# Kernel optimization log

Measured on AMD Instinct MI355X. Metric: run time of the kernel, lower is better.

The kernel has to match this reference:

```python
import jax, jax.numpy as jnp
import numpy as np

B = 32768      # batch size
D = 256        # embedding dim
C = 2048       # number of classes (label range)
WEIGHT = 1.0
TEMPERATURE = 0.3
EPS = 1e-12


def setup_inputs() -> dict:
    key = jax.random.key(0)
    k1, k2 = jax.random.split(key)
    features = jax.random.normal(k1, (B, D), dtype=jnp.float32)
    labels = jax.random.randint(k2, (B,), 0, C, dtype=jnp.int32)
    return {"features": features, "labels": labels, "epoch": 5}


def reference(features, labels, epoch):
    # L2-normalize embeddings (F.normalize, p=2, dim=1)
    norms = jnp.sqrt(jnp.sum(features * features, axis=1, keepdims=True))
    f = features / jnp.maximum(norms, EPS)                      # [B, D]

    # per-class segment sums / counts (vectorized replacement of the python loop)
    ones = jnp.ones((f.shape[0],), dtype=f.dtype)
    counts = jax.ops.segment_sum(ones, labels, num_segments=C)  # [C]
    sums = jax.ops.segment_sum(f, labels, num_segments=C)       # [C, D]
    centroids = sums / jnp.maximum(counts, 1.0)[:, None]        # [C, D] (mean; empty classes masked later)

    # leave-one-out positive centroid: (sum_class - f_i) / (n_class - 1)
    cnt_i = counts[labels]                                       # [B]
    c_p = (sums[labels] - f) / jnp.maximum(cnt_i - 1.0, 1.0)[:, None]
    d_p = jnp.sqrt(jnp.sum((f - c_p) ** 2, axis=1) + EPS)        # [B]

    # distances to all class centroids: ||f||=1 after normalization
    cn2 = jnp.sum(centroids * centroids, axis=1)                 # [C]
    d2 = 1.0 + cn2[None, :] - 2.0 * (f @ centroids.T)           # [B, C]
    d = jnp.sqrt(jnp.maximum(d2, EPS))

    # mask own class and empty (absent-in-batch) classes, take min negative distance
    class_ids = jnp.arange(C, dtype=labels.dtype)
    neg_mask = (counts[None, :] > 0) & (labels[:, None] != class_ids[None, :])
    d_n = jnp.min(jnp.where(neg_mask, d, jnp.inf), axis=1)       # [B]

    # samples are skipped if their class is a singleton or no negative class exists
    valid = (cnt_i > 1.0) & jnp.isfinite(d_n)
    d_n_safe = jnp.where(jnp.isfinite(d_n), d_n, 0.0)

    # temperature schedule: min(temperature + 0.02*epoch, 1)
    temp = min(TEMPERATURE + 0.02 * epoch, 1.0)

    # ln(1 + exp((d_p - d_n)/t)) == softplus
    loss_per_sample = jax.nn.softplus((d_p - d_n_safe) / temp)
    cnt = jnp.sum(valid.astype(f.dtype))
    loss = jnp.where(cnt > 0,
                     jnp.sum(jnp.where(valid, loss_per_sample, 0.0)) / jnp.maximum(cnt, 1.0),
                     0.0)
    return WEIGHT * loss
```

## Files before the change

### kernel.cpp

```cpp
#include <hip/hip_runtime.h>
#include <hip/hip_bf16.h>
#include <math.h>

constexpr int Bn = 32768;
constexpr int Dn = 256;
constexpr int Cn = 2048;
constexpr int NSPLIT = 4;
constexpr int CLS_PER_BLK = Cn / NSPLIT;
constexpr int NIT = CLS_PER_BLK / 16;
#define EPSF 1e-12f
#define INFF __builtin_inff()

typedef __bf16 bf16x8 __attribute__((ext_vector_type(8)));
typedef __bf16 bf16x4 __attribute__((ext_vector_type(4)));
typedef float  f32x4  __attribute__((ext_vector_type(4)));

__device__ inline void async_copy16(const void* g, void* l) {
    __builtin_amdgcn_global_load_lds(
        (const __attribute__((address_space(1))) void*)g,
        (__attribute__((address_space(3))) void*)l, 16, 0, 0);
}

__global__ __launch_bounds__(256) void k_prep(const float* __restrict__ feat,
                                              const int* __restrict__ labels,
                                              __bf16* __restrict__ fneg,
                                              int* __restrict__ hist) {
    const int wave = threadIdx.x >> 6, lane = threadIdx.x & 63;
    const int s = blockIdx.x * 4 + wave;
    const float4 v = ((const float4*)(feat + (size_t)s * Dn))[lane];
    float ss = v.x * v.x + v.y * v.y + v.z * v.z + v.w * v.w;
    #pragma unroll
    for (int off = 1; off < 64; off <<= 1) ss += __shfl_xor(ss, off, 64);
    const float inv = -2.0f / fmaxf(sqrtf(ss), EPSF);
    bf16x4 bf;
    bf[0] = (__bf16)(v.x * inv); bf[1] = (__bf16)(v.y * inv);
    bf[2] = (__bf16)(v.z * inv); bf[3] = (__bf16)(v.w * inv);
    *(bf16x4*)(fneg + (size_t)s * Dn + lane * 4) = bf;
    if (lane == 0) atomicAdd(&hist[labels[s]], 1);
}

__global__ __launch_bounds__(256) void k_scan(const int* __restrict__ hist,
                                              int* __restrict__ cnt_i,
                                              int* __restrict__ offs,
                                              int* __restrict__ offs_work) {
    __shared__ int part[256];
    const int t = threadIdx.x;
    int h[8], pre[8]; int sum = 0;
    #pragma unroll
    for (int j = 0; j < 8; ++j) { h[j] = hist[t * 8 + j]; pre[j] = sum; sum += h[j]; }
    int v = sum;
    part[t] = v; __syncthreads();
    for (int off = 1; off < 256; off <<= 1) {
        int add = (t >= off) ? part[t - off] : 0;
        __syncthreads();
        v += add; part[t] = v;
        __syncthreads();
    }
    const int base = v - sum;
    #pragma unroll
    for (int j = 0; j < 8; ++j) {
        const int b = t * 8 + j, o = base + pre[j];
        cnt_i[b] = h[j]; offs[b] = o; offs_work[b] = o;
    }
}

__global__ __launch_bounds__(256) void k_scatter(const int* __restrict__ labels,
                                                 int* __restrict__ offs_work,
                                                 int* __restrict__ order) {
    const int i = blockIdx.x * 256 + threadIdx.x;
    const int pos = atomicAdd(&offs_work[labels[i]], 1);
    order[pos] = i;
}

__global__ __launch_bounds__(256) void k_centseg(const __bf16* __restrict__ fneg,
                                                 const int* __restrict__ order,
                                                 const int* __restrict__ offs,
                                                 const int* __restrict__ cnt_i,
                                                 __bf16* __restrict__ centK,
                                                 float* __restrict__ cn2x) {
    const int wave = threadIdx.x >> 6, lane = threadIdx.x & 63;
    const int c = blockIdx.x * 4 + wave;
    const int n = cnt_i[c], start = offs[c];
    int myidx = 0;
    if (lane < n) myidx = order[start + lane];
    float sx = 0.f, sy = 0.f, sz = 0.f, sw = 0.f;
    const int nf = (n < 64) ? n : 64;
    for (int j = 0; j < nf; ++j) {
        const int idx = __shfl(myidx, j, 64);
        const bf16x4 v = *(const bf16x4*)(fneg + (size_t)idx * Dn + lane * 4);
        sx += -0.5f * (float)v[0]; sy += -0.5f * (float)v[1];
        sz += -0.5f * (float)v[2]; sw += -0.5f * (float)v[3];
    }
    for (int j = 64; j < n; ++j) {
        const int idx = order[start + j];
        const bf16x4 v = *(const bf16x4*)(fneg + (size_t)idx * Dn + lane * 4);
        sx += -0.5f * (float)v[0]; sy += -0.5f * (float)v[1];
        sz += -0.5f * (float)v[2]; sw += -0.5f * (float)v[3];
    }
    const float invn = 1.0f / fmaxf((float)n, 1.0f);
    const float cx = sx * invn, cy = sy * invn, cz = sz * invn, cw = sw * invn;
    bf16x4 cb; cb[0] = (__bf16)cx; cb[1] = (__bf16)cy; cb[2] = (__bf16)cz; cb[3] = (__bf16)cw;
    *(bf16x4*)(centK + ((size_t)(lane >> 1) * Cn + c) * 8 + (lane & 1) * 4) = cb;
    float ss = cx * cx + cy * cy + cz * cz + cw * cw;
    #pragma unroll
    for (int off = 1; off < 64; off <<= 1) ss += __shfl_xor(ss, off, 64);
    if (lane == 0) cn2x[c] = (n > 0) ? ss : INFF;
}

__global__ __launch_bounds__(256, 2) void k_main(const __bf16* __restrict__ fneg,
                                                 const int* __restrict__ labels,
                                                 const __bf16* __restrict__ centK,
                                                 const float* __restrict__ cn2x,
                                                 float* __restrict__ minval,
                                                 float* __restrict__ dotown) {
    __shared__ __align__(16) __bf16 sB[2][16 * Dn];
    __shared__ float s_cn2[CLS_PER_BLK];
    const int lane = threadIdx.x & 63, wave = threadIdx.x >> 6;
    const int m16 = lane & 15, quad = lane >> 4;
    const int sbase = blockIdx.x * 256 + wave * 64;
    const int c_begin = blockIdx.y * CLS_PER_BLK;

    bf16x8 a[4][8];
    #pragma unroll
    for (int p = 0; p < 4; ++p) {
        const __bf16* fr = fneg + (size_t)(sbase + p * 16 + m16) * Dn + quad * 8;
        #pragma unroll
        for (int t = 0; t < 8; ++t) a[p][t] = *(const bf16x8*)(fr + t * 32);
    }
    int lab[4][4];
    #pragma unroll
    for (int p = 0; p < 4; ++p)
        #pragma unroll
        for (int r = 0; r < 4; ++r)
            lab[p][r] = labels[sbase + p * 16 + quad * 4 + r];

    float rm[4][4], dacc[4][4];
    #pragma unroll
    for (int p = 0; p < 4; ++p)
        #pragma unroll
        for (int r = 0; r < 4; ++r) { rm[p][r] = INFF; dacc[p][r] = 0.0f; }

    auto stage = [&](int buf, int it) {
        const int c0 = c_begin + it * 16;
        #pragma unroll
        for (int j = 0; j < 2; ++j) {
            const int chunk = wave * 128 + j * 64 + lane;
            const int kc = chunk >> 4, n = chunk & 15;
            const __bf16* g = centK + ((size_t)kc * Cn + (c0 + n)) * 8;
            __bf16* l = &sB[buf][(size_t)(wave * 128 + j * 64) * 8];
            async_copy16(g, l);
        }
    };

    stage(0, 0);
    for (int c = threadIdx.x; c < CLS_PER_BLK; c += 256) s_cn2[c] = cn2x[c_begin + c];
    __syncthreads();
    for (int it = 0; it < NIT; ++it) {
        const int cur = it & 1;
        if (it + 1 < NIT) stage(cur ^ 1, it + 1);
        const float cn2v = s_cn2[it * 16 + m16];
        const __bf16* ls = &sB[cur][0];
        f32x4 acc[4] = {{0.f,0.f,0.f,0.f},{0.f,0.f,0.f,0.f},
                        {0.f,0.f,0.f,0.f},{0.f,0.f,0.f,0.f}};
        #pragma unroll
        for (int t = 0; t < 8; ++t) {
            const bf16x8 b = *(const bf16x8*)(ls + t * 512 + lane * 8);
            #pragma unroll
            for (int p = 0; p < 4; ++p)
                acc[p] = __builtin_amdgcn_mfma_f32_16x16x32_bf16(a[p][t], b, acc[p], 0, 0, 0);
        }
        const int crow = c_begin + it * 16 + m16;
        #pragma unroll
        for (int p = 0; p < 4; ++p)
            #pragma unroll
            for (int r = 0; r < 4; ++r) {
                const bool own = (crow == lab[p][r]);
                const float sel = own ? INFF : cn2v;
                rm[p][r] = fminf(rm[p][r], sel + acc[p][r]);
                dacc[p][r] += own ? acc[p][r] : 0.0f;
            }
        __syncthreads();
    }
    #pragma unroll
    for (int off = 1; off < 16; off <<= 1)
        #pragma unroll
        for (int p = 0; p < 4; ++p)
            #pragma unroll
            for (int r = 0; r < 4; ++r) {
                rm[p][r] = fminf(rm[p][r], __shfl_xor(rm[p][r], off, 64));
                dacc[p][r] += __shfl_xor(dacc[p][r], off, 64);
            }
    if (m16 == 0) {
        float* mv = minval + (size_t)blockIdx.y * Bn;
        float* dv = dotown + (size_t)blockIdx.y * Bn;
        #pragma unroll
        for (int p = 0; p < 4; ++p)
            #pragma unroll
            for (int r = 0; r < 4; ++r) {
                mv[sbase + p * 16 + quad * 4 + r] = rm[p][r];
                dv[sbase + p * 16 + quad * 4 + r] = dacc[p][r];
            }
    }
}

__global__ __launch_bounds__(256) void k_final(const int* __restrict__ labels,
                                               const int* __restrict__ cnt_i,
                                               const float* __restrict__ cn2x,
                                               const float* __restrict__ minval,
                                               const float* __restrict__ dotown,
                                               const int* __restrict__ epoch,
                                               float* __restrict__ accum) {
    const int i = blockIdx.x * 256 + threadIdx.x;
    const int lane = threadIdx.x & 63;
    const float temp = fminf(0.3f + 0.02f * (float)(*epoch), 1.0f);
    float m = minval[i];
    float draw = dotown[i];
    #pragma unroll
    for (int k = 1; k < NSPLIT; ++k) {
        m = fminf(m, minval[(size_t)k * Bn + i]);
        draw += dotown[(size_t)k * Bn + i];
    }
    const int l = labels[i];
    const int n = cnt_i[l];
    const float nf = (float)n;
    const float cn2 = cn2x[l];
    const float fds = nf * (-0.5f * draw);
    const float fm1 = fmaxf(nf - 1.0f, 1.0f);
    const float fdcp = (fds - 1.0f) / fm1;
    const float cp2 = (nf * nf * cn2 - 2.0f * fds + 1.0f) / (fm1 * fm1);
    const float dp2 = 1.0f - 2.0f * fdcp + cp2;
    const float d_p = sqrtf(fmaxf(dp2, 0.0f) + EPSF);
    const bool finite = (m < 1e37f);
    const float d_n = finite ? sqrtf(fmaxf(1.0f + m, EPSF)) : 0.0f;
    const bool valid = (n > 1) && finite;
    const float x = (d_p - d_n) / temp;
    const float sp = fmaxf(x, 0.0f) + log1pf(expf(-fabsf(x)));
    float ws = valid ? sp : 0.0f, wc = valid ? 1.0f : 0.0f;
    #pragma unroll
    for (int off = 1; off < 64; off <<= 1) {
        ws += __shfl_xor(ws, off, 64);
        wc += __shfl_xor(wc, off, 64);
    }
    if (lane == 0) {
        atomicAdd(&accum[0], ws);
        atomicAdd(&accum[1], wc);
    }
}

__global__ void k_out(const float* __restrict__ accum, float* __restrict__ out) {
    const float s = accum[0], c = accum[1];
    out[0] = (c > 0.0f) ? (s / fmaxf(c, 1.0f)) : 0.0f;
}

extern "C" void kernel_launch(void* const* d_in, const int* in_sizes, int n_in,
                              void* d_out, int out_size, void* d_ws, size_t ws_size,
                              hipStream_t stream) {
    const float* feat  = (const float*)d_in[0];
    const int* labels  = (const int*)d_in[1];
    const int* epoch   = (const int*)d_in[2];
    float* out = (float*)d_out;
    char* ws = (char*)d_ws;

    size_t off = 0;
    __bf16* fneg     = (__bf16*)(ws + off); off += (size_t)Bn * Dn * 2;
    __bf16* centK    = (__bf16*)(ws + off); off += (size_t)Cn * Dn * 2;
    float*  cn2x     = (float*)(ws + off);  off += (size_t)Cn * 4;
    int*    hist     = (int*)(ws + off);    off += (size_t)Cn * 4;
    int*    cnt_i    = (int*)(ws + off);    off += (size_t)Cn * 4;
    int*    offs     = (int*)(ws + off);    off += (size_t)Cn * 4;
    int*    offs_wk  = (int*)(ws + off);    off += (size_t)Cn * 4;
    int*    order    = (int*)(ws + off);    off += (size_t)Bn * 4;
    float*  minval   = (float*)(ws + off);  off += (size_t)NSPLIT * Bn * 4;
    float*  dotown   = (float*)(ws + off);  off += (size_t)NSPLIT * Bn * 4;
    float*  accum    = (float*)(ws + off);  off += 2 * 4;

    (void)hipMemsetAsync(hist,  0, (size_t)Cn * sizeof(int), stream);
    (void)hipMemsetAsync(accum, 0, 2 * sizeof(float), stream);

    k_prep<<<Bn / 4, 256, 0, stream>>>(feat, labels, fneg, hist);
    k_scan<<<1, 256, 0, stream>>>(hist, cnt_i, offs, offs_wk);
    k_scatter<<<Bn / 256, 256, 0, stream>>>(labels, offs_wk, order);
    k_centseg<<<Cn / 4, 256, 0, stream>>>(fneg, order, offs, cnt_i, centK, cn2x);
    dim3 g5(Bn / 256, NSPLIT);
    k_main<<<g5, 256, 0, stream>>>(fneg, labels, centK, cn2x, minval, dotown);
    k_final<<<Bn / 256, 256, 0, stream>>>(labels, cnt_i, cn2x, minval, dotown,
                                          epoch, accum);
    k_out<<<1, 1, 0, stream>>>(accum, out);
}
```

Measured before the change: 166.2 us.

## Fuse all stages into one cooperative persistent kernel with grid syncs

Replaces the chain of seven kernel launches and two memsets with a single cooperative kernel. The stages are normalize, scan, scatter, centroid, distance GEMM and final reduction, and grid-wide barriers separate them. NSPLIT is also raised to 8 so the persistent grid has more GEMM work units to spread out. This removes launch gaps but adds the cost of grid syncs, and the single-block scan stage leaves the rest of the grid idle. The GEMM stage's occupancy is also limited by the cooperative grid size.

```diff
diff --git a/kernel.cpp b/kernel.cpp
--- a/kernel.cpp
+++ b/kernel.cpp
@@ -1,13 +1,17 @@
 #include <hip/hip_runtime.h>
 #include <hip/hip_bf16.h>
+#include <hip/hip_cooperative_groups.h>
 #include <math.h>
+
+namespace cg = cooperative_groups;
 
 constexpr int Bn = 32768;
 constexpr int Dn = 256;
 constexpr int Cn = 2048;
-constexpr int NSPLIT = 4;
+constexpr int NSPLIT = 8;
 constexpr int CLS_PER_BLK = Cn / NSPLIT;
 constexpr int NIT = CLS_PER_BLK / 16;
+constexpr int NU = (Bn / 256) * NSPLIT;
 #define EPSF 1e-12f
 #define INFF __builtin_inff()
 
@@ -21,235 +25,236 @@
         (__attribute__((address_space(3))) void*)l, 16, 0, 0);
 }
 
-__global__ __launch_bounds__(256) void k_prep(const float* __restrict__ feat,
-                                              const int* __restrict__ labels,
-                                              __bf16* __restrict__ fneg,
-                                              int* __restrict__ hist) {
-    const int wave = threadIdx.x >> 6, lane = threadIdx.x & 63;
-    const int s = blockIdx.x * 4 + wave;
-    const float4 v = ((const float4*)(feat + (size_t)s * Dn))[lane];
-    float ss = v.x * v.x + v.y * v.y + v.z * v.z + v.w * v.w;
-    #pragma unroll
-    for (int off = 1; off < 64; off <<= 1) ss += __shfl_xor(ss, off, 64);
-    const float inv = -2.0f / fmaxf(sqrtf(ss), EPSF);
-    bf16x4 bf;
-    bf[0] = (__bf16)(v.x * inv); bf[1] = (__bf16)(v.y * inv);
-    bf[2] = (__bf16)(v.z * inv); bf[3] = (__bf16)(v.w * inv);
-    *(bf16x4*)(fneg + (size_t)s * Dn + lane * 4) = bf;
-    if (lane == 0) atomicAdd(&hist[labels[s]], 1);
-}
-
-__global__ __launch_bounds__(256) void k_scan(const int* __restrict__ hist,
-                                              int* __restrict__ cnt_i,
-                                              int* __restrict__ offs,
-                                              int* __restrict__ offs_work) {
-    __shared__ int part[256];
-    const int t = threadIdx.x;
-    int h[8], pre[8]; int sum = 0;
-    #pragma unroll
-    for (int j = 0; j < 8; ++j) { h[j] = hist[t * 8 + j]; pre[j] = sum; sum += h[j]; }
-    int v = sum;
-    part[t] = v; __syncthreads();
-    for (int off = 1; off < 256; off <<= 1) {
-        int add = (t >= off) ? part[t - off] : 0;
-        __syncthreads();
-        v += add; part[t] = v;
-        __syncthreads();
-    }
-    const int base = v - sum;
-    #pragma unroll
-    for (int j = 0; j < 8; ++j) {
-        const int b = t * 8 + j, o = base + pre[j];
-        cnt_i[b] = h[j]; offs[b] = o; offs_work[b] = o;
-    }
-}
-
-__global__ __launch_bounds__(256) void k_scatter(const int* __restrict__ labels,
-                                                 int* __restrict__ offs_work,
-                                                 int* __restrict__ order) {
-    const int i = blockIdx.x * 256 + threadIdx.x;
-    const int pos = atomicAdd(&offs_work[labels[i]], 1);
-    order[pos] = i;
-}
-
-__global__ __launch_bounds__(256) void k_centseg(const __bf16* __restrict__ fneg,
-                                                 const int* __restrict__ order,
-                                                 const int* __restrict__ offs,
-                                                 const int* __restrict__ cnt_i,
-                                                 __bf16* __restrict__ centK,
-                                                 float* __restrict__ cn2x) {
-    const int wave = threadIdx.x >> 6, lane = threadIdx.x & 63;
-    const int c = blockIdx.x * 4 + wave;
-    const int n = cnt_i[c], start = offs[c];
-    int myidx = 0;
-    if (lane < n) myidx = order[start + lane];
-    float sx = 0.f, sy = 0.f, sz = 0.f, sw = 0.f;
-    const int nf = (n < 64) ? n : 64;
-    for (int j = 0; j < nf; ++j) {
-        const int idx = __shfl(myidx, j, 64);
-        const bf16x4 v = *(const bf16x4*)(fneg + (size_t)idx * Dn + lane * 4);
-        sx += -0.5f * (float)v[0]; sy += -0.5f * (float)v[1];
-        sz += -0.5f * (float)v[2]; sw += -0.5f * (float)v[3];
-    }
-    for (int j = 64; j < n; ++j) {
-        const int idx = order[start + j];
-        const bf16x4 v = *(const bf16x4*)(fneg + (size_t)idx * Dn + lane * 4);
-        sx += -0.5f * (float)v[0]; sy += -0.5f * (float)v[1];
-        sz += -0.5f * (float)v[2]; sw += -0.5f * (float)v[3];
-    }
-    const float invn = 1.0f / fmaxf((float)n, 1.0f);
-    const float cx = sx * invn, cy = sy * invn, cz = sz * invn, cw = sw * invn;
-    bf16x4 cb; cb[0] = (__bf16)cx; cb[1] = (__bf16)cy; cb[2] = (__bf16)cz; cb[3] = (__bf16)cw;
-    *(bf16x4*)(centK + ((size_t)(lane >> 1) * Cn + c) * 8 + (lane & 1) * 4) = cb;
-    float ss = cx * cx + cy * cy + cz * cz + cw * cw;
-    #pragma unroll
-    for (int off = 1; off < 64; off <<= 1) ss += __shfl_xor(ss, off, 64);
-    if (lane == 0) cn2x[c] = (n > 0) ? ss : INFF;
-}
-
-__global__ __launch_bounds__(256, 2) void k_main(const __bf16* __restrict__ fneg,
-                                                 const int* __restrict__ labels,
-                                                 const __bf16* __restrict__ centK,
-                                                 const float* __restrict__ cn2x,
-                                                 float* __restrict__ minval,
-                                                 float* __restrict__ dotown) {
+__global__ __launch_bounds__(256, 2) void k_fused(
+    const float* __restrict__ feat, const int* __restrict__ labels,
+    const int* __restrict__ epoch,
+    __bf16* fneg, int* hist, int* cnt_i, int* offs, int* offs_wk, int* order,
+    __bf16* centK, float* cn2x, float* minval, float* dotown,
+    float* accum, float* out)
+{
     __shared__ __align__(16) __bf16 sB[2][16 * Dn];
     __shared__ float s_cn2[CLS_PER_BLK];
-    const int lane = threadIdx.x & 63, wave = threadIdx.x >> 6;
+    __shared__ int s_part[256];
+
+    cg::grid_group gg = cg::this_grid();
+    const int tid = threadIdx.x;
+    const int gtid = blockIdx.x * 256 + tid;
+    const int nthreads = gridDim.x * 256;
+    const int nwaves = nthreads >> 6;
+    const int wave_id = gtid >> 6;
+    const int lane = tid & 63;
+    const int wave = tid >> 6;
+
+    for (int c = gtid; c < Cn; c += nthreads) hist[c] = 0;
+    if (gtid < 2) accum[gtid] = 0.0f;
+    gg.sync();
+
+    for (int s = wave_id; s < Bn; s += nwaves) {
+        const float4 v = ((const float4*)(feat + (size_t)s * Dn))[lane];
+        float ss = v.x * v.x + v.y * v.y + v.z * v.z + v.w * v.w;
+        #pragma unroll
+        for (int off = 1; off < 64; off <<= 1) ss += __shfl_xor(ss, off, 64);
+        const float inv = -2.0f / fmaxf(sqrtf(ss), EPSF);
+        bf16x4 bf;
+        bf[0] = (__bf16)(v.x * inv); bf[1] = (__bf16)(v.y * inv);
+        bf[2] = (__bf16)(v.z * inv); bf[3] = (__bf16)(v.w * inv);
+        *(bf16x4*)(fneg + (size_t)s * Dn + lane * 4) = bf;
+        if (lane == 0) atomicAdd(&hist[labels[s]], 1);
+    }
+    gg.sync();
+
+    if (blockIdx.x == 0) {
+        int h[8], pre[8]; int sum = 0;
+        #pragma unroll
+        for (int j = 0; j < 8; ++j) { h[j] = hist[tid * 8 + j]; pre[j] = sum; sum += h[j]; }
+        int v = sum;
+        s_part[tid] = v; __syncthreads();
+        for (int off = 1; off < 256; off <<= 1) {
+            int add = (tid >= off) ? s_part[tid - off] : 0;
+            __syncthreads();
+            v += add; s_part[tid] = v;
+            __syncthreads();
+        }
+        const int base = v - sum;
+        #pragma unroll
+        for (int j = 0; j < 8; ++j) {
+            const int b = tid * 8 + j, o = base + pre[j];
+            cnt_i[b] = h[j]; offs[b] = o; offs_wk[b] = o;
+        }
+    }
+    gg.sync();
+
+    for (int i = gtid; i < Bn; i += nthreads) {
+        const int pos = atomicAdd(&offs_wk[labels[i]], 1);
+        order[pos] = i;
+    }
+    gg.sync();
+
+    for (int c = wave_id; c < Cn; c += nwaves) {
+        const int n = cnt_i[c], start = offs[c];
+        int myidx = 0;
+        if (lane < n) myidx = order[start + lane];
+        float sx = 0.f, sy = 0.f, sz = 0.f, sw = 0.f;
+        const int nf = (n < 64) ? n : 64;
+        for (int j = 0; j < nf; ++j) {
+            const int idx = __shfl(myidx, j, 64);
+            const bf16x4 v = *(const bf16x4*)(fneg + (size_t)idx * Dn + lane * 4);
+            sx += -0.5f * (float)v[0]; sy += -0.5f * (float)v[1];
+            sz += -0.5f * (float)v[2]; sw += -0.5f * (float)v[3];
+        }
+        for (int j = 64; j < n; ++j) {
+            const int idx = order[start + j];
+            const bf16x4 v = *(const bf16x4*)(fneg + (size_t)idx * Dn + lane * 4);
+            sx += -0.5f * (float)v[0]; sy += -0.5f * (float)v[1];
+            sz += -0.5f * (float)v[2]; sw += -0.5f * (float)v[3];
+        }
+        const float invn = 1.0f / fmaxf((float)n, 1.0f);
+        const float cx = sx * invn, cy = sy * invn, cz = sz * invn, cw = sw * invn;
+        bf16x4 cb; cb[0] = (__bf16)cx; cb[1] = (__bf16)cy;
+        cb[2] = (__bf16)cz; cb[3] = (__bf16)cw;
+        *(bf16x4*)(centK + ((size_t)(lane >> 1) * Cn + c) * 8 + (lane & 1) * 4) = cb;
+        float ss = cx * cx + cy * cy + cz * cz + cw * cw;
+        #pragma unroll
+        for (int off = 1; off < 64; off <<= 1) ss += __shfl_xor(ss, off, 64);
+        if (lane == 0) cn2x[c] = (n > 0) ? ss : INFF;
+    }
+    gg.sync();
+
     const int m16 = lane & 15, quad = lane >> 4;
-    const int sbase = blockIdx.x * 256 + wave * 64;
-    const int c_begin = blockIdx.y * CLS_PER_BLK;
-
-    bf16x8 a[4][8];
-    #pragma unroll
-    for (int p = 0; p < 4; ++p) {
-        const __bf16* fr = fneg + (size_t)(sbase + p * 16 + m16) * Dn + quad * 8;
-        #pragma unroll
-        for (int t = 0; t < 8; ++t) a[p][t] = *(const bf16x8*)(fr + t * 32);
-    }
-    int lab[4][4];
-    #pragma unroll
-    for (int p = 0; p < 4; ++p)
-        #pragma unroll
-        for (int r = 0; r < 4; ++r)
-            lab[p][r] = labels[sbase + p * 16 + quad * 4 + r];
-
-    float rm[4][4], dacc[4][4];
-    #pragma unroll
-    for (int p = 0; p < 4; ++p)
-        #pragma unroll
-        for (int r = 0; r < 4; ++r) { rm[p][r] = INFF; dacc[p][r] = 0.0f; }
-
-    auto stage = [&](int buf, int it) {
-        const int c0 = c_begin + it * 16;
-        #pragma unroll
-        for (int j = 0; j < 2; ++j) {
-            const int chunk = wave * 128 + j * 64 + lane;
-            const int kc = chunk >> 4, n = chunk & 15;
-            const __bf16* g = centK + ((size_t)kc * Cn + (c0 + n)) * 8;
-            __bf16* l = &sB[buf][(size_t)(wave * 128 + j * 64) * 8];
-            async_copy16(g, l);
-        }
-    };
-
-    stage(0, 0);
-    for (int c = threadIdx.x; c < CLS_PER_BLK; c += 256) s_cn2[c] = cn2x[c_begin + c];
-    __syncthreads();
-    for (int it = 0; it < NIT; ++it) {
-        const int cur = it & 1;
-        if (it + 1 < NIT) stage(cur ^ 1, it + 1);
-        const float cn2v = s_cn2[it * 16 + m16];
-        const __bf16* ls = &sB[cur][0];
-        f32x4 acc[4] = {{0.f,0.f,0.f,0.f},{0.f,0.f,0.f,0.f},
-                        {0.f,0.f,0.f,0.f},{0.f,0.f,0.f,0.f}};
-        #pragma unroll
-        for (int t = 0; t < 8; ++t) {
-            const bf16x8 b = *(const bf16x8*)(ls + t * 512 + lane * 8);
+    for (int u = blockIdx.x; u < NU; u += gridDim.x) {
+        const int bx = u & 127, by = u >> 7;
+        const int sbase = bx * 256 + wave * 64;
+        const int c_begin = by * CLS_PER_BLK;
+
+        bf16x8 a[4][8];
+        #pragma unroll
+        for (int p = 0; p < 4; ++p) {
+            const __bf16* fr = fneg + (size_t)(sbase + p * 16 + m16) * Dn + quad * 8;
+            #pragma unroll
+            for (int t = 0; t < 8; ++t) a[p][t] = *(const bf16x8*)(fr + t * 32);
+        }
+        int lab[4][4];
+        #pragma unroll
+        for (int p = 0; p < 4; ++p)
+            #pragma unroll
+            for (int r = 0; r < 4; ++r)
+                lab[p][r] = labels[sbase + p * 16 + quad * 4 + r];
+
+        float rm[4][4], dacc[4][4];
+        #pragma unroll
+        for (int p = 0; p < 4; ++p)
+            #pragma unroll
+            for (int r = 0; r < 4; ++r) { rm[p][r] = INFF; dacc[p][r] = 0.0f; }
+
+        auto stage = [&](int buf, int it) {
+            const int c0 = c_begin + it * 16;
+            #pragma unroll
+            for (int j = 0; j < 2; ++j) {
+                const int chunk = wave * 128 + j * 64 + lane;
+                const int kc = chunk >> 4, n = chunk & 15;
+                const __bf16* g = centK + ((size_t)kc * Cn + (c0 + n)) * 8;
+                __bf16* l = &sB[buf][(size_t)(wave * 128 + j * 64) * 8];
+                async_copy16(g, l);
+            }
+        };
+
+        stage(0, 0);
+        for (int c = tid; c < CLS_PER_BLK; c += 256) s_cn2[c] = cn2x[c_begin + c];
+        __syncthreads();
+        for (int it = 0; it < NIT; ++it) {
+            const int cur = it & 1;
+            if (it + 1 < NIT) stage(cur ^ 1, it + 1);
+            const float cn2v = s_cn2[it * 16 + m16];
+            const __bf16* ls = &sB[cur][0];
+            f32x4 acc[4] = {{0.f,0.f,0.f,0.f},{0.f,0.f,0.f,0.f},
+                            {0.f,0.f,0.f,0.f},{0.f,0.f,0.f,0.f}};
+            #pragma unroll
+            for (int t = 0; t < 8; ++t) {
+                const bf16x8 b = *(const bf16x8*)(ls + t * 512 + lane * 8);
+                #pragma unroll
+                for (int p = 0; p < 4; ++p)
+                    acc[p] = __builtin_amdgcn_mfma_f32_16x16x32_bf16(a[p][t], b, acc[p], 0, 0, 0);
+            }
+            const int crow = c_begin + it * 16 + m16;
             #pragma unroll
             for (int p = 0; p < 4; ++p)
-                acc[p] = __builtin_amdgcn_mfma_f32_16x16x32_bf16(a[p][t], b, acc[p], 0, 0, 0);
-        }
-        const int crow = c_begin + it * 16 + m16;
-        #pragma unroll
-        for (int p = 0; p < 4; ++p)
-            #pragma unroll
-            for (int r = 0; r < 4; ++r) {
-                const bool own = (crow == lab[p][r]);
-                const float sel = own ? INFF : cn2v;
-                rm[p][r] = fminf(rm[p][r], sel + acc[p][r]);
-                dacc[p][r] += own ? acc[p][r] : 0.0f;
+                #pragma unroll
+                for (int r = 0; r < 4; ++r) {
+                    const bool own = (crow == lab[p][r]);
+                    const float sel = own ? INFF : cn2v;
+                    rm[p][r] = fminf(rm[p][r], sel + acc[p][r]);
+                    dacc[p][r] += own ? acc[p][r] : 0.0f;
+                }
+            __syncthreads();
+        }
+        #pragma unroll
+        for (int off = 1; off < 16; off <<= 1)
+            #pragma unroll
+            for (int p = 0; p < 4; ++p)
+                #pragma unroll
+                for (int r = 0; r < 4; ++r) {
+                    rm[p][r] = fminf(rm[p][r], __shfl_xor(rm[p][r], off, 64));
+                    dacc[p][r] += __shfl_xor(dacc[p][r], off, 64);
+                }
+        if (m16 == 0) {
+            float* mv = minval + (size_t)by * Bn;
+            float* dv = dotown + (size_t)by * Bn;
+            #pragma unroll
+            for (int p = 0; p < 4; ++p)
+                #pragma unroll
+                for (int r = 0; r < 4; ++r) {
+                    mv[sbase + p * 16 + quad * 4 + r] = rm[p][r];
+                    dv[sbase + p * 16 + quad * 4 + r] = dacc[p][r];
+                }
+        }
+    }
+    gg.sync();
+
+    {
+        const float temp = fminf(0.3f + 0.02f * (float)(*epoch), 1.0f);
+        float ws = 0.0f, wc = 0.0f;
+        for (int i = gtid; i < Bn; i += nthreads) {
+            float m = minval[i];
+            float draw = dotown[i];
+            #pragma unroll
+            for (int k = 1; k < NSPLIT; ++k) {
+                m = fminf(m, minval[(size_t)k * Bn + i]);
+                draw += dotown[(size_t)k * Bn + i];
             }
-        __syncthreads();
-    }
-    #pragma unroll
-    for (int off = 1; off < 16; off <<= 1)
-        #pragma unroll
-        for (int p = 0; p < 4; ++p)
-            #pragma unroll
-            for (int r = 0; r < 4; ++r) {
-                rm[p][r] = fminf(rm[p][r], __shfl_xor(rm[p][r], off, 64));
-                dacc[p][r] += __shfl_xor(dacc[p][r], off, 64);
-            }
-    if (m16 == 0) {
-        float* mv = minval + (size_t)blockIdx.y * Bn;
-        float* dv = dotown + (size_t)blockIdx.y * Bn;
-        #pragma unroll
-        for (int p = 0; p < 4; ++p)
-            #pragma unroll
-            for (int r = 0; r < 4; ++r) {
-                mv[sbase + p * 16 + quad * 4 + r] = rm[p][r];
-                dv[sbase + p * 16 + quad * 4 + r] = dacc[p][r];
-            }
-    }
-}
-
-__global__ __launch_bounds__(256) void k_final(const int* __restrict__ labels,
-                                               const int* __restrict__ cnt_i,
-                                               const float* __restrict__ cn2x,
-                                               const float* __restrict__ minval,
-                                               const float* __restrict__ dotown,
-                                               const int* __restrict__ epoch,
-                                               float* __restrict__ accum) {
-    const int i = blockIdx.x * 256 + threadIdx.x;
-    const int lane = threadIdx.x & 63;
-    const float temp = fminf(0.3f + 0.02f * (float)(*epoch), 1.0f);
-    float m = minval[i];
-    float draw = dotown[i];
-    #pragma unroll
-    for (int k = 1; k < NSPLIT; ++k) {
-        m = fminf(m, minval[(size_t)k * Bn + i]);
-        draw += dotown[(size_t)k * Bn + i];
-    }
-    const int l = labels[i];
-    const int n = cnt_i[l];
-    const float nf = (float)n;
-    const float cn2 = cn2x[l];
-    const float fds = nf * (-0.5f * draw);
-    const float fm1 = fmaxf(nf - 1.0f, 1.0f);
-    const float fdcp = (fds - 1.0f) / fm1;
-    const float cp2 = (nf * nf * cn2 - 2.0f * fds + 1.0f) / (fm1 * fm1);
-    const float dp2 = 1.0f - 2.0f * fdcp + cp2;
-    const float d_p = sqrtf(fmaxf(dp2, 0.0f) + EPSF);
-    const bool finite = (m < 1e37f);
-    const float d_n = finite ? sqrtf(fmaxf(1.0f + m, EPSF)) : 0.0f;
-    const bool valid = (n > 1) && finite;
-    const float x = (d_p - d_n) / temp;
-    const float sp = fmaxf(x, 0.0f) + log1pf(expf(-fabsf(x)));
-    float ws = valid ? sp : 0.0f, wc = valid ? 1.0f : 0.0f;
-    #pragma unroll
-    for (int off = 1; off < 64; off <<= 1) {
-        ws += __shfl_xor(ws, off, 64);
-        wc += __shfl_xor(wc, off, 64);
-    }
-    if (lane == 0) {
-        atomicAdd(&accum[0], ws);
-        atomicAdd(&accum[1], wc);
-    }
-}
-
-__global__ void k_out(const float* __restrict__ accum, float* __restrict__ out) {
-    const float s = accum[0], c = accum[1];
-    out[0] = (c > 0.0f) ? (s / fmaxf(c, 1.0f)) : 0.0f;
+            const int l = labels[i];
+            const int n = cnt_i[l];
+            const float nf = (float)n;
+            const float cn2 = cn2x[l];
+            const float fds = nf * (-0.5f * draw);
+            const float fm1 = fmaxf(nf - 1.0f, 1.0f);
+            const float fdcp = (fds - 1.0f) / fm1;
+            const float cp2 = (nf * nf * cn2 - 2.0f * fds + 1.0f) / (fm1 * fm1);
+            const float dp2 = 1.0f - 2.0f * fdcp + cp2;
+            const float d_p = sqrtf(fmaxf(dp2, 0.0f) + EPSF);
+            const bool finite = (m < 1e37f);
+            const float d_n = finite ? sqrtf(fmaxf(1.0f + m, EPSF)) : 0.0f;
+            const bool valid = (n > 1) && finite;
+            const float x = (d_p - d_n) / temp;
+            const float sp = fmaxf(x, 0.0f) + log1pf(expf(-fabsf(x)));
+            ws += valid ? sp : 0.0f;
+            wc += valid ? 1.0f : 0.0f;
+        }
+        #pragma unroll
+        for (int off = 1; off < 64; off <<= 1) {
+            ws += __shfl_xor(ws, off, 64);
+            wc += __shfl_xor(wc, off, 64);
+        }
+        if (lane == 0) {
+            atomicAdd(&accum[0], ws);
+            atomicAdd(&accum[1], wc);
+        }
+    }
+    gg.sync();
+
+    if (gtid == 0) {
+        const float s = accum[0], c = accum[1];
+        out[0] = (c > 0.0f) ? (s / fmaxf(c, 1.0f)) : 0.0f;
+    }
 }
 
 extern "C" void kernel_launch(void* const* d_in, const int* in_sizes, int n_in,
@@ -262,28 +267,29 @@
     char* ws = (char*)d_ws;
 
     size_t off = 0;
-    __bf16* fneg     = (__bf16*)(ws + off); off += (size_t)Bn * Dn * 2;
-    __bf16* centK    = (__bf16*)(ws + off); off += (size_t)Cn * Dn * 2;
-    float*  cn2x     = (float*)(ws + off);  off += (size_t)Cn * 4;
-    int*    hist     = (int*)(ws + off);    off += (size_t)Cn * 4;
-    int*    cnt_i    = (int*)(ws + off);    off += (size_t)Cn * 4;
-    int*    offs     = (int*)(ws + off);    off += (size_t)Cn * 4;
-    int*    offs_wk  = (int*)(ws + off);    off += (size_t)Cn * 4;
-    int*    order    = (int*)(ws + off);    off += (size_t)Bn * 4;
-    float*  minval   = (float*)(ws + off);  off += (size_t)NSPLIT * Bn * 4;
-    float*  dotown   = (float*)(ws + off);  off += (size_t)NSPLIT * Bn * 4;
-    float*  accum    = (float*)(ws + off);  off += 2 * 4;
-
-    (void)hipMemsetAsync(hist,  0, (size_t)Cn * sizeof(int), stream);
-    (void)hipMemsetAsync(accum, 0, 2 * sizeof(float), stream);
-
-    k_prep<<<Bn / 4, 256, 0, stream>>>(feat, labels, fneg, hist);
-    k_scan<<<1, 256, 0, stream>>>(hist, cnt_i, offs, offs_wk);
-    k_scatter<<<Bn / 256, 256, 0, stream>>>(labels, offs_wk, order);
-    k_centseg<<<Cn / 4, 256, 0, stream>>>(fneg, order, offs, cnt_i, centK, cn2x);
-    dim3 g5(Bn / 256, NSPLIT);
-    k_main<<<g5, 256, 0, stream>>>(fneg, labels, centK, cn2x, minval, dotown);
-    k_final<<<Bn / 256, 256, 0, stream>>>(labels, cnt_i, cn2x, minval, dotown,
-                                          epoch, accum);
-    k_out<<<1, 1, 0, stream>>>(accum, out);
+    __bf16* fneg   = (__bf16*)(ws + off); off += (size_t)Bn * Dn * 2;
+    __bf16* centK  = (__bf16*)(ws + off); off += (size_t)Cn * Dn * 2;
+    float*  cn2x   = (float*)(ws + off);  off += (size_t)Cn * 4;
+    int*    hist   = (int*)(ws + off);    off += (size_t)Cn * 4;
+    int*    cnt_i  = (int*)(ws + off);    off += (size_t)Cn * 4;
+    int*    offsp  = (int*)(ws + off);    off += (size_t)Cn * 4;
+    int*    offs_wk= (int*)(ws + off);    off += (size_t)Cn * 4;
+    int*    order  = (int*)(ws + off);    off += (size_t)Bn * 4;
+    float*  minval = (float*)(ws + off);  off += (size_t)NSPLIT * Bn * 4;
+    float*  dotown = (float*)(ws + off);  off += (size_t)NSPLIT * Bn * 4;
+    float*  accum  = (float*)(ws + off);  off += 2 * 4;
+
+    int maxb = 0;
+    if (hipOccupancyMaxActiveBlocksPerMultiprocessor(
+            &maxb, (const void*)k_fused, 256, 0) != hipSuccess || maxb < 1)
+        maxb = 1;
+    int grid = maxb * 256;
+    if (grid > 1024) grid = 1024;
+
+    void* args[] = {(void*)&feat, (void*)&labels, (void*)&epoch,
+                    (void*)&fneg, (void*)&hist, (void*)&cnt_i, (void*)&offsp,
+                    (void*)&offs_wk, (void*)&order, (void*)&centK, (void*)&cn2x,
+                    (void*)&minval, (void*)&dotown, (void*)&accum, (void*)&out};
+    (void)hipLaunchCooperativeKernel((const void*)k_fused, dim3(grid), dim3(256),
+                                     args, 0, stream);
 }
```

Result: slower. 404.7 us (+143.6%).

## Fuse scan and output into last-block epilogues; stage 32 classes per iteration

Applied to the files above, without the earlier changes.

Folds the single-block histogram scan into k_prep through a last-block ticket, and the final output division into k_final the same way. This removes two tiny kernel launches and merges the two memsets into one. k_main now stages 32 classes per double-buffered step instead of 16, halving the number of barriers and stage calls. In exchange it doubles LDS per block, which may affect occupancy, and depends on atomic ticket ordering and threadfence for correctness.

```diff
diff --git a/kernel.cpp b/kernel.cpp
--- a/kernel.cpp
+++ b/kernel.cpp
@@ -7,7 +7,7 @@
 constexpr int Cn = 2048;
 constexpr int NSPLIT = 4;
 constexpr int CLS_PER_BLK = Cn / NSPLIT;
-constexpr int NIT = CLS_PER_BLK / 16;
+constexpr int NSUP = CLS_PER_BLK / 32;
 #define EPSF 1e-12f
 #define INFF __builtin_inff()
 
@@ -24,8 +24,13 @@
 __global__ __launch_bounds__(256) void k_prep(const float* __restrict__ feat,
                                               const int* __restrict__ labels,
                                               __bf16* __restrict__ fneg,
-                                              int* __restrict__ hist) {
-    const int wave = threadIdx.x >> 6, lane = threadIdx.x & 63;
+                                              int* __restrict__ hist,
+                                              int* __restrict__ cnt_i,
+                                              int* __restrict__ offs,
+                                              int* __restrict__ offs_wk,
+                                              int* __restrict__ ticket) {
+    const int tid = threadIdx.x;
+    const int wave = tid >> 6, lane = tid & 63;
     const int s = blockIdx.x * 4 + wave;
     const float4 v = ((const float4*)(feat + (size_t)s * Dn))[lane];
     float ss = v.x * v.x + v.y * v.y + v.z * v.z + v.w * v.w;
@@ -37,30 +42,35 @@
     bf[2] = (__bf16)(v.z * inv); bf[3] = (__bf16)(v.w * inv);
     *(bf16x4*)(fneg + (size_t)s * Dn + lane * 4) = bf;
     if (lane == 0) atomicAdd(&hist[labels[s]], 1);
-}
-
-__global__ __launch_bounds__(256) void k_scan(const int* __restrict__ hist,
-                                              int* __restrict__ cnt_i,
-                                              int* __restrict__ offs,
-                                              int* __restrict__ offs_work) {
-    __shared__ int part[256];
-    const int t = threadIdx.x;
+
+    __shared__ int s_part[256];
+    __shared__ int s_last;
+    __syncthreads();
+    if (tid == 0) {
+        __threadfence();
+        s_last = (atomicAdd(ticket, 1) == (int)gridDim.x - 1) ? 1 : 0;
+    }
+    __syncthreads();
+    if (!s_last) return;
     int h[8], pre[8]; int sum = 0;
     #pragma unroll
-    for (int j = 0; j < 8; ++j) { h[j] = hist[t * 8 + j]; pre[j] = sum; sum += h[j]; }
-    int v = sum;
-    part[t] = v; __syncthreads();
+    for (int j = 0; j < 8; ++j) {
+        h[j] = atomicAdd(&hist[tid * 8 + j], 0);
+        pre[j] = sum; sum += h[j];
+    }
+    int vv = sum;
+    s_part[tid] = vv; __syncthreads();
     for (int off = 1; off < 256; off <<= 1) {
-        int add = (t >= off) ? part[t - off] : 0;
+        int add = (tid >= off) ? s_part[tid - off] : 0;
         __syncthreads();
-        v += add; part[t] = v;
+        vv += add; s_part[tid] = vv;
         __syncthreads();
     }
-    const int base = v - sum;
+    const int base = vv - sum;
     #pragma unroll
     for (int j = 0; j < 8; ++j) {
-        const int b = t * 8 + j, o = base + pre[j];
-        cnt_i[b] = h[j]; offs[b] = o; offs_work[b] = o;
+        const int b = tid * 8 + j, o = base + pre[j];
+        cnt_i[b] = h[j]; offs[b] = o; offs_wk[b] = o;
     }
 }
 
@@ -99,7 +109,8 @@
     }
     const float invn = 1.0f / fmaxf((float)n, 1.0f);
     const float cx = sx * invn, cy = sy * invn, cz = sz * invn, cw = sw * invn;
-    bf16x4 cb; cb[0] = (__bf16)cx; cb[1] = (__bf16)cy; cb[2] = (__bf16)cz; cb[3] = (__bf16)cw;
+    bf16x4 cb; cb[0] = (__bf16)cx; cb[1] = (__bf16)cy;
+    cb[2] = (__bf16)cz; cb[3] = (__bf16)cw;
     *(bf16x4*)(centK + ((size_t)(lane >> 1) * Cn + c) * 8 + (lane & 1) * 4) = cb;
     float ss = cx * cx + cy * cy + cz * cz + cw * cw;
     #pragma unroll
@@ -113,7 +124,7 @@
                                                  const float* __restrict__ cn2x,
                                                  float* __restrict__ minval,
                                                  float* __restrict__ dotown) {
-    __shared__ __align__(16) __bf16 sB[2][16 * Dn];
+    __shared__ __align__(16) __bf16 sB[2][32 * Dn];
     __shared__ float s_cn2[CLS_PER_BLK];
     const int lane = threadIdx.x & 63, wave = threadIdx.x >> 6;
     const int m16 = lane & 15, quad = lane >> 4;
@@ -140,14 +151,14 @@
         #pragma unroll
         for (int r = 0; r < 4; ++r) { rm[p][r] = INFF; dacc[p][r] = 0.0f; }
 
-    auto stage = [&](int buf, int it) {
-        const int c0 = c_begin + it * 16;
-        #pragma unroll
-        for (int j = 0; j < 2; ++j) {
-            const int chunk = wave * 128 + j * 64 + lane;
-            const int kc = chunk >> 4, n = chunk & 15;
-            const __bf16* g = centK + ((size_t)kc * Cn + (c0 + n)) * 8;
-            __bf16* l = &sB[buf][(size_t)(wave * 128 + j * 64) * 8];
+    auto stage = [&](int buf, int s) {
+        const int c0 = c_begin + s * 32;
+        #pragma unroll
+        for (int j = 0; j < 4; ++j) {
+            const int L = wave * 256 + j * 64 + lane;
+            const int st = L >> 9, kc = (L >> 4) & 31, n = L & 15;
+            const __bf16* g = centK + ((size_t)kc * Cn + (c0 + st * 16 + n)) * 8;
+            __bf16* l = &sB[buf][(size_t)(wave * 256 + j * 64) * 8];
             async_copy16(g, l);
         }
     };
@@ -155,30 +166,33 @@
     stage(0, 0);
     for (int c = threadIdx.x; c < CLS_PER_BLK; c += 256) s_cn2[c] = cn2x[c_begin + c];
     __syncthreads();
-    for (int it = 0; it < NIT; ++it) {
-        const int cur = it & 1;
-        if (it + 1 < NIT) stage(cur ^ 1, it + 1);
-        const float cn2v = s_cn2[it * 16 + m16];
-        const __bf16* ls = &sB[cur][0];
-        f32x4 acc[4] = {{0.f,0.f,0.f,0.f},{0.f,0.f,0.f,0.f},
-                        {0.f,0.f,0.f,0.f},{0.f,0.f,0.f,0.f}};
-        #pragma unroll
-        for (int t = 0; t < 8; ++t) {
-            const bf16x8 b = *(const bf16x8*)(ls + t * 512 + lane * 8);
+    for (int s = 0; s < NSUP; ++s) {
+        const int cur = s & 1;
+        if (s + 1 < NSUP) stage(cur ^ 1, s + 1);
+        #pragma unroll
+        for (int st = 0; st < 2; ++st) {
+            const float cn2v = s_cn2[s * 32 + st * 16 + m16];
+            const __bf16* ls = &sB[cur][st * 4096];
+            f32x4 acc[4] = {{0.f,0.f,0.f,0.f},{0.f,0.f,0.f,0.f},
+                            {0.f,0.f,0.f,0.f},{0.f,0.f,0.f,0.f}};
+            #pragma unroll
+            for (int t = 0; t < 8; ++t) {
+                const bf16x8 b = *(const bf16x8*)(ls + t * 512 + lane * 8);
+                #pragma unroll
+                for (int p = 0; p < 4; ++p)
+                    acc[p] = __builtin_amdgcn_mfma_f32_16x16x32_bf16(a[p][t], b, acc[p], 0, 0, 0);
+            }
+            const int crow = c_begin + s * 32 + st * 16 + m16;
             #pragma unroll
             for (int p = 0; p < 4; ++p)
-                acc[p] = __builtin_amdgcn_mfma_f32_16x16x32_bf16(a[p][t], b, acc[p], 0, 0, 0);
+                #pragma unroll
+                for (int r = 0; r < 4; ++r) {
+                    const bool own = (crow == lab[p][r]);
+                    const float sel = own ? INFF : cn2v;
+                    rm[p][r] = fminf(rm[p][r], sel + acc[p][r]);
+                    dacc[p][r] += own ? acc[p][r] : 0.0f;
+                }
         }
-        const int crow = c_begin + it * 16 + m16;
-        #pragma unroll
-        for (int p = 0; p < 4; ++p)
-            #pragma unroll
-            for (int r = 0; r < 4; ++r) {
-                const bool own = (crow == lab[p][r]);
-                const float sel = own ? INFF : cn2v;
-                rm[p][r] = fminf(rm[p][r], sel + acc[p][r]);
-                dacc[p][r] += own ? acc[p][r] : 0.0f;
-            }
         __syncthreads();
     }
     #pragma unroll
@@ -209,9 +223,12 @@
                                                const float* __restrict__ minval,
                                                const float* __restrict__ dotown,
                                                const int* __restrict__ epoch,
-                                               float* __restrict__ accum) {
-    const int i = blockIdx.x * 256 + threadIdx.x;
-    const int lane = threadIdx.x & 63;
+                                               float* __restrict__ accum,
+                                               int* __restrict__ ticket,
+                                               float* __restrict__ out) {
+    const int tid = threadIdx.x;
+    const int i = blockIdx.x * 256 + tid;
+    const int lane = tid & 63;
     const float temp = fminf(0.3f + 0.02f * (float)(*epoch), 1.0f);
     float m = minval[i];
     float draw = dotown[i];
@@ -245,11 +262,18 @@
         atomicAdd(&accum[0], ws);
         atomicAdd(&accum[1], wc);
     }
-}
-
-__global__ void k_out(const float* __restrict__ accum, float* __restrict__ out) {
-    const float s = accum[0], c = accum[1];
-    out[0] = (c > 0.0f) ? (s / fmaxf(c, 1.0f)) : 0.0f;
+    __shared__ int s_last;
+    __syncthreads();
+    if (tid == 0) {
+        __threadfence();
+        s_last = (atomicAdd(ticket, 1) == (int)gridDim.x - 1) ? 1 : 0;
+    }
+    __syncthreads();
+    if (s_last && tid == 0) {
+        const float s = atomicAdd(&accum[0], 0.0f);
+        const float c = atomicAdd(&accum[1], 0.0f);
+        out[0] = (c > 0.0f) ? (s / fmaxf(c, 1.0f)) : 0.0f;
+    }
 }
 
 extern "C" void kernel_launch(void* const* d_in, const int* in_sizes, int n_in,
@@ -262,28 +286,27 @@
     char* ws = (char*)d_ws;
 
     size_t off = 0;
-    __bf16* fneg     = (__bf16*)(ws + off); off += (size_t)Bn * Dn * 2;
-    __bf16* centK    = (__bf16*)(ws + off); off += (size_t)Cn * Dn * 2;
-    float*  cn2x     = (float*)(ws + off);  off += (size_t)Cn * 4;
-    int*    hist     = (int*)(ws + off);    off += (size_t)Cn * 4;
-    int*    cnt_i    = (int*)(ws + off);    off += (size_t)Cn * 4;
-    int*    offs     = (int*)(ws + off);    off += (size_t)Cn * 4;
-    int*    offs_wk  = (int*)(ws + off);    off += (size_t)Cn * 4;
-    int*    order    = (int*)(ws + off);    off += (size_t)Bn * 4;
-    float*  minval   = (float*)(ws + off);  off += (size_t)NSPLIT * Bn * 4;
-    float*  dotown   = (float*)(ws + off);  off += (size_t)NSPLIT * Bn * 4;
-    float*  accum    = (float*)(ws + off);  off += 2 * 4;
-
-    (void)hipMemsetAsync(hist,  0, (size_t)Cn * sizeof(int), stream);
-    (void)hipMemsetAsync(accum, 0, 2 * sizeof(float), stream);
-
-    k_prep<<<Bn / 4, 256, 0, stream>>>(feat, labels, fneg, hist);
-    k_scan<<<1, 256, 0, stream>>>(hist, cnt_i, offs, offs_wk);
+    __bf16* fneg   = (__bf16*)(ws + off); off += (size_t)Bn * Dn * 2;
+    __bf16* centK  = (__bf16*)(ws + off); off += (size_t)Cn * Dn * 2;
+    float*  cn2x   = (float*)(ws + off);  off += (size_t)Cn * 4;
+    int*    cnt_i  = (int*)(ws + off);    off += (size_t)Cn * 4;
+    int*    offsp  = (int*)(ws + off);    off += (size_t)Cn * 4;
+    int*    offs_wk= (int*)(ws + off);    off += (size_t)Cn * 4;
+    int*    order  = (int*)(ws + off);    off += (size_t)Bn * 4;
+    float*  minval = (float*)(ws + off);  off += (size_t)NSPLIT * Bn * 4;
+    float*  dotown = (float*)(ws + off);  off += (size_t)NSPLIT * Bn * 4;
+    int*    hist   = (int*)(ws + off);    off += (size_t)Cn * 4;
+    float*  accum  = (float*)(ws + off);  off += 2 * 4;
+    int*    ticket = (int*)(ws + off);    off += 2 * 4;
+
+    (void)hipMemsetAsync(hist, 0, (size_t)Cn * 4 + 16, stream);
+
+    k_prep<<<Bn / 4, 256, 0, stream>>>(feat, labels, fneg, hist, cnt_i, offsp,
+                                       offs_wk, &ticket[0]);
     k_scatter<<<Bn / 256, 256, 0, stream>>>(labels, offs_wk, order);
-    k_centseg<<<Cn / 4, 256, 0, stream>>>(fneg, order, offs, cnt_i, centK, cn2x);
-    dim3 g5(Bn / 256, NSPLIT);
-    k_main<<<g5, 256, 0, stream>>>(fneg, labels, centK, cn2x, minval, dotown);
+    k_centseg<<<Cn / 4, 256, 0, stream>>>(fneg, order, offsp, cnt_i, centK, cn2x);
+    dim3 g4(Bn / 256, NSPLIT);
+    k_main<<<g4, 256, 0, stream>>>(fneg, labels, centK, cn2x, minval, dotown);
     k_final<<<Bn / 256, 256, 0, stream>>>(labels, cnt_i, cn2x, minval, dotown,
-                                          epoch, accum);
-    k_out<<<1, 1, 0, stream>>>(accum, out);
-}
+                                          epoch, accum, &ticket[1], out);
+}
```

Result: slower. 344.7 us (+107.4%).
